# Kernel tuning notes

Hardware: AMD Instinct MI355X
Metric: run time of the kernel (lower is better)

## Reference

```python
import jax, jax.numpy as jnp
import numpy as np

N, E = 100000, 1600000
IN_DIM, EDGE_DIM, H, D = 128, 16, 8, 16
SLOPE = 0.2


def setup_inputs() -> dict:
    key = jax.random.key(0)
    k1, k2, k3, k4, k5, k6, k7 = jax.random.split(key, 7)
    node_embeddings = jax.random.normal(k1, (N, IN_DIM), dtype=jnp.float32)
    edge_index = jax.random.randint(k2, (2, E), 0, N, dtype=jnp.int64)
    edge_features = jax.random.normal(k3, (E, EDGE_DIM), dtype=jnp.float32)
    # xavier_uniform with gain 1/sqrt(2) for linear weights (shape [out, in])
    g = 1.0 / np.sqrt(2.0)
    b_node = g * np.sqrt(6.0 / (IN_DIM + H * D))
    W_node = jax.random.uniform(k4, (H * D, IN_DIM), jnp.float32, -b_node, b_node)
    b_edge = g * np.sqrt(6.0 / (EDGE_DIM + H * D))
    W_edge = jax.random.uniform(k5, (H * D, EDGE_DIM), jnp.float32, -b_edge, b_edge)
    # xavier on attn_vec.unsqueeze(0): fan_in = 3D, fan_out = H*3D? torch treats
    # (1, H, 3D) as fan_in=3D, fan_out=H*3D is not standard; torch uses last dim as fan_in,
    # dims[-2]=H as fan_out for 3D tensors with receptive field 1 -> fan_in=3D, fan_out=H.
    b_a = np.sqrt(6.0 / (H + 3 * D))
    attn_vec = jax.random.uniform(k6, (H, 3 * D), jnp.float32, -b_a, b_a)
    return {
        "node_embeddings": node_embeddings,
        "edge_features": edge_features,
        "W_node": W_node,
        "W_edge": W_edge,
        "attn_vec": attn_vec,
        "edge_index": edge_index,
    }


def _leaky_relu(x, slope=SLOPE):
    return jnp.where(x >= 0, x, slope * x)


def reference(node_embeddings, edge_features, W_node, W_edge, attn_vec, edge_index):
    n = node_embeddings.shape[0]
    src, dst = edge_index[0], edge_index[1]
    h = (node_embeddings @ W_node.T).reshape(n, H, D)           # (N,H,D)
    ef = (edge_features @ W_edge.T).reshape(-1, H, D)           # (E,H,D)
    a_src, a_dst, a_edge = attn_vec[:, :D], attn_vec[:, D:2 * D], attn_vec[:, 2 * D:]
    # split the dot product: a^T [h_src || h_dst || e] = a1.h_src + a2.h_dst + a3.e
    s_node_src = jnp.einsum('nhd,hd->nh', h, a_src)             # (N,H)
    s_node_dst = jnp.einsum('nhd,hd->nh', h, a_dst)             # (N,H)
    score = s_node_src[src] + s_node_dst[dst] + jnp.einsum('ehd,hd->eh', ef, a_edge)
    score = _leaky_relu(score)                                  # (E,H)
    # torch scatter_reduce amax with include_self=True on zeros init => max(seg_max, 0)
    seg_max = jnp.maximum(jax.ops.segment_max(score, dst, num_segments=n), 0.0)  # (N,H)
    exp_s = jnp.exp(score - seg_max[dst])                       # (E,H)
    denom = jax.ops.segment_sum(exp_s, dst, num_segments=n)     # (N,H)
    w = exp_s / (denom[dst] + 1e-9)                             # (E,H)  (dropout in eval mode)
    msg = h[src] * w[:, :, None]                                # (E,H,D)
    out = jax.ops.segment_sum(msg, dst, num_segments=n)         # (N,H,D)
    return jax.nn.elu(out).reshape(n, H * D)
```

## Files before the change

### kernel.cpp

```cpp
#include <hip/hip_runtime.h>
#include <hip/hip_bf16.h>
#include <hip/hip_fp16.h>
#include <math.h>

#define NN 100000
#define NE 1600000
#define SLOPE 0.2f
#define BSH 9
#define NB 196
#define BCAP 10240
#define CLDS 10752
#define EPB 4096
#define NTB 64

typedef float  f32x4 __attribute__((ext_vector_type(4)));
typedef unsigned int u32x4 __attribute__((ext_vector_type(4)));
typedef _Float16 half8 __attribute__((ext_vector_type(8)));
typedef float floatx4 __attribute__((ext_vector_type(4)));

__global__ __launch_bounds__(128) void prep_v_kernel(
    const float* __restrict__ W_edge, const float* __restrict__ attn,
    float* __restrict__ v)
{
    int t = threadIdx.x;
    int h = t >> 4, k = t & 15;
    float acc = 0.f;
#pragma unroll
    for (int d = 0; d < 16; ++d)
        acc += attn[h * 48 + 32 + d] * W_edge[(h * 16 + d) * 16 + k];
    v[t] = acc;
}

__global__ __launch_bounds__(256) void node_transform(
    const float* __restrict__ X, const float* __restrict__ Wn,
    const float* __restrict__ attn, __half* __restrict__ h_fp,
    float* __restrict__ s_src, float* __restrict__ s_dst)
{
    __shared__ _Float16 Wl[128 * 128];

    int t = threadIdx.x;
#pragma unroll
    for (int it = 0; it < 8; ++it) {
        int gid = t + it * 256;
        int j  = gid >> 4;
        int gk = gid & 15;
        const float4* wp = reinterpret_cast<const float4*>(Wn + (size_t)j * 128 + gk * 8);
        float4 w0 = wp[0], w1 = wp[1];
        half8 hw;
        hw[0] = (_Float16)w0.x; hw[1] = (_Float16)w0.y;
        hw[2] = (_Float16)w0.z; hw[3] = (_Float16)w0.w;
        hw[4] = (_Float16)w1.x; hw[5] = (_Float16)w1.y;
        hw[6] = (_Float16)w1.z; hw[7] = (_Float16)w1.w;
        int sg = gk ^ (j & 7);
        *reinterpret_cast<half8*>(&Wl[j * 128 + sg * 8]) = hw;
    }
    __syncthreads();

    int lane = t & 63;
    int wave = t >> 6;
    int c = lane & 15;
    int g = lane >> 4;
    int n0 = blockIdx.x * NTB + wave * 16;
    if (n0 >= NN) return;

    floatx4 acc[8];
#pragma unroll
    for (int jt = 0; jt < 8; ++jt) acc[jt] = (floatx4){0.f, 0.f, 0.f, 0.f};

    const float4* xrow = reinterpret_cast<const float4*>(X + (size_t)(n0 + c) * 128);
#pragma unroll
    for (int kb = 0; kb < 4; ++kb) {
        float4 x0 = xrow[kb * 8 + g * 2];
        float4 x1 = xrow[kb * 8 + g * 2 + 1];
        half8 a;
        a[0] = (_Float16)x0.x; a[1] = (_Float16)x0.y;
        a[2] = (_Float16)x0.z; a[3] = (_Float16)x0.w;
        a[4] = (_Float16)x1.x; a[5] = (_Float16)x1.y;
        a[6] = (_Float16)x1.z; a[7] = (_Float16)x1.w;
#pragma unroll
        for (int jt = 0; jt < 8; ++jt) {
            int sg = (kb * 4 + g) ^ (c & 7);
            half8 b = *reinterpret_cast<const half8*>(&Wl[(jt * 16 + c) * 128 + sg * 8]);
            acc[jt] = __builtin_amdgcn_mfma_f32_16x16x32_f16(a, b, acc[jt], 0, 0, 0);
        }
    }

    float as_l[8], ad_l[8];
#pragma unroll
    for (int jt = 0; jt < 8; ++jt) {
        as_l[jt] = attn[jt * 48 + c];
        ad_l[jt] = attn[jt * 48 + 16 + c];
    }

#pragma unroll
    for (int jt = 0; jt < 8; ++jt) {
#pragma unroll
        for (int r = 0; r < 4; ++r) {
            float hv = acc[jt][r];
            int node = n0 + g * 4 + r;
            h_fp[(size_t)node * 128 + jt * 16 + c] = __float2half_rn(hv);
            float p1 = hv * as_l[jt];
            float p2 = hv * ad_l[jt];
#pragma unroll
            for (int m = 1; m < 16; m <<= 1) {
                p1 += __shfl_xor(p1, m);
                p2 += __shfl_xor(p2, m);
            }
            if (c == 0) {
                s_src[(size_t)node * 8 + jt] = p1;
                s_dst[(size_t)node * 8 + jt] = p2;
            }
        }
    }
}

__global__ __launch_bounds__(256) void edge_score_partition(
    const int* __restrict__ ei, const float* __restrict__ ef,
    const float* __restrict__ vglob, const float* __restrict__ s_src,
    const float* __restrict__ s_dst, unsigned int* __restrict__ bcursor,
    u32x4* __restrict__ esc4, u32x4* __restrict__ esc_s,
    int2* __restrict__ brec)
{
    __shared__ float v[128];
    __shared__ unsigned int hist[256];
    __shared__ unsigned int runstart[256];
    __shared__ unsigned int cursor[256];
    __shared__ unsigned int gbase[NB];
    __shared__ int           sdst[EPB];
    __shared__ int           ssin[EPB];
    __shared__ unsigned int  skey[EPB];
    __shared__ unsigned int  ssrc[EPB];
    __shared__ unsigned short sbkt[EPB];

    int t = threadIdx.x;
    int e0 = blockIdx.x * EPB;
    int ecnt = min(EPB, NE - e0);

    if (t < 128) v[t] = vglob[t];
    hist[t] = 0;
    __syncthreads();

    const f32x4* ef4 = reinterpret_cast<const f32x4*>(ef);
    const float4* ss4 = reinterpret_cast<const float4*>(s_src);
    const float4* sd4 = reinterpret_cast<const float4*>(s_dst);

    for (int i = t; i < ecnt; i += 256) {
        int e = e0 + i;
        int src = ei[e];
        int dst = ei[NE + e];
        sdst[i] = dst;
        ssin[i] = src;
        atomicAdd(&hist[dst >> BSH], 1u);

        float tt[8] = {0.f, 0.f, 0.f, 0.f, 0.f, 0.f, 0.f, 0.f};
#pragma unroll
        for (int r = 0; r < 4; ++r) {
            f32x4 fv = ef4[(size_t)e * 4 + r];
#pragma unroll
            for (int hh = 0; hh < 8; ++hh) {
                tt[hh] += fv[0] * v[hh * 16 + r * 4 + 0]
                        + fv[1] * v[hh * 16 + r * 4 + 1]
                        + fv[2] * v[hh * 16 + r * 4 + 2]
                        + fv[3] * v[hh * 16 + r * 4 + 3];
            }
        }
        float4 a0 = ss4[(size_t)src * 2], a1 = ss4[(size_t)src * 2 + 1];
        float4 b0 = sd4[(size_t)dst * 2], b1 = sd4[(size_t)dst * 2 + 1];
        float sa[8] = {a0.x, a0.y, a0.z, a0.w, a1.x, a1.y, a1.z, a1.w};
        float sb[8] = {b0.x, b0.y, b0.z, b0.w, b1.x, b1.y, b1.z, b1.w};
        u32x4 pk4;
#pragma unroll
        for (int hp = 0; hp < 4; ++hp) {
            unsigned int lohi[2];
#pragma unroll
            for (int half_ = 0; half_ < 2; ++half_) {
                int hh = hp * 2 + half_;
                float s = sa[hh] + sb[hh] + tt[hh];
                s = (s >= 0.f) ? s : SLOPE * s;
                lohi[half_] = (unsigned int)__half_as_ushort(__float2half_rn(__expf(s)));
            }
            pk4[hp] = lohi[0] | (lohi[1] << 16);
        }
        esc4[e] = pk4;
    }
    __syncthreads();

    unsigned int hv = hist[t];
    runstart[t] = hv;
    __syncthreads();
    for (int o = 1; o < 256; o <<= 1) {
        unsigned int u = (t >= o) ? runstart[t - o] : 0u;
        __syncthreads();
        runstart[t] += u;
        __syncthreads();
    }
    unsigned int excl = runstart[t] - hv;
    __syncthreads();
    runstart[t] = excl;
    cursor[t] = excl;
    if (t < NB) gbase[t] = atomicAdd(&bcursor[t], hv);
    __syncthreads();

    for (int i = t; i < ecnt; i += 256) {
        int e = e0 + i;
        int dst = sdst[i];
        int b = dst >> BSH;
        unsigned int slot = atomicAdd(&cursor[b], 1u);
        skey[slot] = ((unsigned int)e << BSH) | (unsigned int)(dst & 511);
        ssrc[slot] = (unsigned int)ssin[i];
        sbkt[slot] = (unsigned short)b;
    }
    __syncthreads();

    for (int s = t; s < ecnt; s += 256) {
        int b = sbkt[s];
        unsigned int gpos = gbase[b] + ((unsigned int)s - runstart[b]);
        if (gpos < BCAP) {
            unsigned int key = skey[s];
            unsigned int e = key >> BSH;
            brec[(size_t)b * BCAP + gpos] =
                make_int2((int)((gpos << BSH) | (key & 511u)), (int)ssrc[s]);
            esc_s[(size_t)b * BCAP + gpos] = esc4[e];
        }
    }
}

__global__ __launch_bounds__(512) void bucket_sort(
    const unsigned int* __restrict__ bcursor, int2* __restrict__ brec,
    uint2* __restrict__ noff)
{
    __shared__ unsigned int ncnt[512];
    __shared__ unsigned int offL[513];
    __shared__ unsigned int ncur[512];
    __shared__ unsigned int se[CLDS];
    __shared__ unsigned int ss[CLDS];

    int t = threadIdx.x;
    int b = blockIdx.x;
    int n0 = b << BSH;
    unsigned int cnt = bcursor[b];
    if (cnt > BCAP) cnt = BCAP;
    int2* rin = brec + (size_t)b * BCAP;

    ncnt[t] = 0;
    __syncthreads();
    for (unsigned int i = t; i < cnt; i += 512)
        atomicAdd(&ncnt[(unsigned int)rin[i].x & 511u], 1u);
    __syncthreads();
    unsigned int ec = (ncnt[t] + 1u) & ~1u;
    offL[t] = ec;
    __syncthreads();
    for (int o = 1; o < 512; o <<= 1) {
        unsigned int u = (t >= o) ? offL[t - o] : 0u;
        __syncthreads();
        offL[t] += u;
        __syncthreads();
    }
    unsigned int incl = offL[t];
    unsigned int excl = incl - ec;
    __syncthreads();
    offL[t] = excl;
    ncur[t] = 0;
    if (t == 511) offL[512] = incl;
    __syncthreads();
    for (unsigned int i = t; i < cnt; i += 512) {
        int2 r = rin[i];
        unsigned int key = (unsigned int)r.x;
        unsigned int ld = key & 511u;
        unsigned int pos = atomicAdd(&ncur[ld], 1u);
        unsigned int slot = offL[ld] + pos;
        if (slot < CLDS) {
            se[slot] = key >> BSH;
            ss[slot] = (unsigned int)r.y;
        }
    }
    __syncthreads();
    unsigned int total = offL[512];
    if (total > BCAP) total = BCAP;
    for (unsigned int s = t; s < total; s += 512)
        rin[s] = make_int2((int)se[s], (int)ss[s]);
    int n = n0 + t;
    if (n < NN)
        noff[n] = make_uint2((unsigned int)b * BCAP + offL[t], ncnt[t]);
}

__global__ __launch_bounds__(256) void node_aggregate(
    const uint2* __restrict__ noff, const int2* __restrict__ perm2,
    const __half* __restrict__ esc_s, const __half* __restrict__ h_fp,
    float* __restrict__ out)
{
    int lane = threadIdx.x & 63;
    int n = blockIdx.x * (blockDim.x >> 6) + (threadIdx.x >> 6);
    if (n >= NN) return;
    int q = lane >> 3;
    const unsigned int* hl = reinterpret_cast<const unsigned int*>(h_fp) + lane;
    const __half* el = esc_s + ((size_t)(n >> BSH) * BCAP) * 8 + q;

    uint2 oc = noff[n];
    unsigned int s0 = oc.x, s1 = s0 + oc.y;
    float denom = 0.f, a0 = 0.f, a1 = 0.f;
    unsigned int i = s0;

    for (; i + 8 <= s1; i += 8) {
        int4 pa = *reinterpret_cast<const int4*>(&perm2[i]);
        int4 pb = *reinterpret_cast<const int4*>(&perm2[i + 2]);
        int4 pc = *reinterpret_cast<const int4*>(&perm2[i + 4]);
        int4 pd = *reinterpret_cast<const int4*>(&perm2[i + 6]);
        unsigned int u0 = hl[(size_t)pa.y * 64];
        unsigned int u1 = hl[(size_t)pa.w * 64];
        unsigned int u2 = hl[(size_t)pb.y * 64];
        unsigned int u3 = hl[(size_t)pb.w * 64];
        unsigned int u4 = hl[(size_t)pc.y * 64];
        unsigned int u5 = hl[(size_t)pc.w * 64];
        unsigned int u6 = hl[(size_t)pd.y * 64];
        unsigned int u7 = hl[(size_t)pd.w * 64];
        float e0 = __half2float(el[(size_t)pa.x * 8]);
        float e1 = __half2float(el[(size_t)pa.z * 8]);
        float e2 = __half2float(el[(size_t)pb.x * 8]);
        float e3 = __half2float(el[(size_t)pb.z * 8]);
        float e4 = __half2float(el[(size_t)pc.x * 8]);
        float e5 = __half2float(el[(size_t)pc.z * 8]);
        float e6 = __half2float(el[(size_t)pd.x * 8]);
        float e7 = __half2float(el[(size_t)pd.z * 8]);
        float2 h0 = __half22float2(*reinterpret_cast<const __half2*>(&u0));
        float2 h1 = __half22float2(*reinterpret_cast<const __half2*>(&u1));
        float2 h2 = __half22float2(*reinterpret_cast<const __half2*>(&u2));
        float2 h3 = __half22float2(*reinterpret_cast<const __half2*>(&u3));
        float2 h4 = __half22float2(*reinterpret_cast<const __half2*>(&u4));
        float2 h5 = __half22float2(*reinterpret_cast<const __half2*>(&u5));
        float2 h6 = __half22float2(*reinterpret_cast<const __half2*>(&u6));
        float2 h7 = __half22float2(*reinterpret_cast<const __half2*>(&u7));
        denom += ((e0 + e1) + (e2 + e3)) + ((e4 + e5) + (e6 + e7));
        a0 = fmaf(h0.x, e0, a0); a0 = fmaf(h1.x, e1, a0);
        a0 = fmaf(h2.x, e2, a0); a0 = fmaf(h3.x, e3, a0);
        a0 = fmaf(h4.x, e4, a0); a0 = fmaf(h5.x, e5, a0);
        a0 = fmaf(h6.x, e6, a0); a0 = fmaf(h7.x, e7, a0);
        a1 = fmaf(h0.y, e0, a1); a1 = fmaf(h1.y, e1, a1);
        a1 = fmaf(h2.y, e2, a1); a1 = fmaf(h3.y, e3, a1);
        a1 = fmaf(h4.y, e4, a1); a1 = fmaf(h5.y, e5, a1);
        a1 = fmaf(h6.y, e6, a1); a1 = fmaf(h7.y, e7, a1);
    }
    for (; i + 4 <= s1; i += 4) {
        int4 pa = *reinterpret_cast<const int4*>(&perm2[i]);
        int4 pb = *reinterpret_cast<const int4*>(&perm2[i + 2]);
        unsigned int u0 = hl[(size_t)pa.y * 64];
        unsigned int u1 = hl[(size_t)pa.w * 64];
        unsigned int u2 = hl[(size_t)pb.y * 64];
        unsigned int u3 = hl[(size_t)pb.w * 64];
        float e0 = __half2float(el[(size_t)pa.x * 8]);
        float e1 = __half2float(el[(size_t)pa.z * 8]);
        float e2 = __half2float(el[(size_t)pb.x * 8]);
        float e3 = __half2float(el[(size_t)pb.z * 8]);
        float2 h0 = __half22float2(*reinterpret_cast<const __half2*>(&u0));
        float2 h1 = __half22float2(*reinterpret_cast<const __half2*>(&u1));
        float2 h2 = __half22float2(*reinterpret_cast<const __half2*>(&u2));
        float2 h3 = __half22float2(*reinterpret_cast<const __half2*>(&u3));
        denom += (e0 + e1) + (e2 + e3);
        a0 = fmaf(h0.x, e0, a0); a0 = fmaf(h1.x, e1, a0);
        a0 = fmaf(h2.x, e2, a0); a0 = fmaf(h3.x, e3, a0);
        a1 = fmaf(h0.y, e0, a1); a1 = fmaf(h1.y, e1, a1);
        a1 = fmaf(h2.y, e2, a1); a1 = fmaf(h3.y, e3, a1);
    }
    for (; i < s1; ++i) {
        int2 p = perm2[i];
        unsigned int u = hl[(size_t)p.y * 64];
        float e = __half2float(el[(size_t)p.x * 8]);
        float2 hf = __half22float2(*reinterpret_cast<const __half2*>(&u));
        denom += e;
        a0 = fmaf(hf.x, e, a0);
        a1 = fmaf(hf.y, e, a1);
    }

    float w = 1.f / (denom + 1e-9f);
    a0 *= w; a1 *= w;
    a0 = a0 > 0.f ? a0 : expm1f(a0);
    a1 = a1 > 0.f ? a1 : expm1f(a1);
    reinterpret_cast<float2*>(out)[(size_t)n * 64 + lane] = make_float2(a0, a1);
}

extern "C" void kernel_launch(void* const* d_in, const int* in_sizes, int n_in,
                              void* d_out, int out_size, void* d_ws, size_t ws_size,
                              hipStream_t stream)
{
    const float* X    = (const float*)d_in[0];
    const float* EF   = (const float*)d_in[1];
    const float* Wn   = (const float*)d_in[2];
    const float* We   = (const float*)d_in[3];
    const float* attn = (const float*)d_in[4];
    const int*   ei   = (const int*)d_in[5];
    float* out = (float*)d_out;

    char* ws = (char*)d_ws;
    int2*   brec  = (int2*)ws;
    u32x4*  esc4  = (u32x4*)(brec + (size_t)NB * BCAP);
    u32x4*  esc_s = esc4 + NE;
    float*  s_src = (float*)(esc_s + (size_t)NB * BCAP);
    float*  s_dst = s_src + (size_t)NN * 8;
    float*  vbuf  = s_dst + (size_t)NN * 8;
    unsigned int* bcursor = (unsigned int*)(vbuf + 128);
    uint2*  noff  = (uint2*)(bcursor + 256);
    __half* h_fp  = (__half*)(noff + NN);

    hipMemsetAsync(bcursor, 0, 256 * sizeof(unsigned int), stream);

    prep_v_kernel<<<1, 128, 0, stream>>>(We, attn, vbuf);
    node_transform<<<(NN + NTB - 1) / NTB, 256, 0, stream>>>(X, Wn, attn, h_fp,
                                                             s_src, s_dst);
    edge_score_partition<<<(NE + EPB - 1) / EPB, 256, 0, stream>>>(
        ei, EF, vbuf, s_src, s_dst, bcursor, esc4, esc_s, brec);
    bucket_sort<<<NB, 512, 0, stream>>>(bcursor, brec, noff);
    node_aggregate<<<(NN + 3) / 4, 256, 0, stream>>>(noff, brec,
                                                     (const __half*)esc_s,
                                                     h_fp, out);
}
```

Before: 224.5 us.

## Compute bucket slots before scoring and write scores directly to bucketed positions

Edge-score partitioning now builds the histogram and prefix scan before computing scores. Each edge grabs its bucket slot via an LDS atomic, and its packed fp16 scores are written straight into the bucketed esc_s array. This removes the intermediate esc4 buffer (a 16-byte store plus a later gather read per edge) and the LDS staging of sorted keys. The trade-off is that edge index reads and score computation fall into separate passes, and the output writes within each bucket are less contiguous than the old slot-ordered scatter.

```diff
diff --git a/kernel.cpp b/kernel.cpp
--- a/kernel.cpp
+++ b/kernel.cpp
@@ -118,8 +118,7 @@
     const int* __restrict__ ei, const float* __restrict__ ef,
     const float* __restrict__ vglob, const float* __restrict__ s_src,
     const float* __restrict__ s_dst, unsigned int* __restrict__ bcursor,
-    u32x4* __restrict__ esc4, u32x4* __restrict__ esc_s,
-    int2* __restrict__ brec)
+    u32x4* __restrict__ esc_s, int2* __restrict__ brec)
 {
     __shared__ float v[128];
     __shared__ unsigned int hist[256];
@@ -128,9 +127,6 @@
     __shared__ unsigned int gbase[NB];
     __shared__ int           sdst[EPB];
     __shared__ int           ssin[EPB];
-    __shared__ unsigned int  skey[EPB];
-    __shared__ unsigned int  ssrc[EPB];
-    __shared__ unsigned short sbkt[EPB];
 
     int t = threadIdx.x;
     int e0 = blockIdx.x * EPB;
@@ -140,17 +136,46 @@
     hist[t] = 0;
     __syncthreads();
 
+    for (int i = t; i < ecnt; i += 256) {
+        int src = ei[e0 + i];
+        int dst = ei[NE + e0 + i];
+        sdst[i] = dst;
+        ssin[i] = src;
+        atomicAdd(&hist[dst >> BSH], 1u);
+    }
+    __syncthreads();
+
+    unsigned int hv = hist[t];
+    runstart[t] = hv;
+    __syncthreads();
+    for (int o = 1; o < 256; o <<= 1) {
+        unsigned int u = (t >= o) ? runstart[t - o] : 0u;
+        __syncthreads();
+        runstart[t] += u;
+        __syncthreads();
+    }
+    unsigned int excl = runstart[t] - hv;
+    __syncthreads();
+    runstart[t] = excl;
+    cursor[t] = excl;
+    if (t < NB) gbase[t] = atomicAdd(&bcursor[t], hv);
+    __syncthreads();
+
     const f32x4* ef4 = reinterpret_cast<const f32x4*>(ef);
     const float4* ss4 = reinterpret_cast<const float4*>(s_src);
     const float4* sd4 = reinterpret_cast<const float4*>(s_dst);
 
     for (int i = t; i < ecnt; i += 256) {
         int e = e0 + i;
-        int src = ei[e];
-        int dst = ei[NE + e];
-        sdst[i] = dst;
-        ssin[i] = src;
-        atomicAdd(&hist[dst >> BSH], 1u);
+        int dst = sdst[i];
+        int src = ssin[i];
+        int b = dst >> BSH;
+        unsigned int slot = atomicAdd(&cursor[b], 1u);
+        unsigned int gp = gbase[b] + (slot - runstart[b]);
+        bool ok = (gp < BCAP);
+        if (ok)
+            brec[(size_t)b * BCAP + gp] =
+                make_int2((int)((gp << BSH) | (unsigned int)(dst & 511)), src);
 
         float tt[8] = {0.f, 0.f, 0.f, 0.f, 0.f, 0.f, 0.f, 0.f};
 #pragma unroll
@@ -181,47 +206,8 @@
             }
             pk4[hp] = lohi[0] | (lohi[1] << 16);
         }
-        esc4[e] = pk4;
-    }
-    __syncthreads();
-
-    unsigned int hv = hist[t];
-    runstart[t] = hv;
-    __syncthreads();
-    for (int o = 1; o < 256; o <<= 1) {
-        unsigned int u = (t >= o) ? runstart[t - o] : 0u;
-        __syncthreads();
-        runstart[t] += u;
-        __syncthreads();
-    }
-    unsigned int excl = runstart[t] - hv;
-    __syncthreads();
-    runstart[t] = excl;
-    cursor[t] = excl;
-    if (t < NB) gbase[t] = atomicAdd(&bcursor[t], hv);
-    __syncthreads();
-
-    for (int i = t; i < ecnt; i += 256) {
-        int e = e0 + i;
-        int dst = sdst[i];
-        int b = dst >> BSH;
-        unsigned int slot = atomicAdd(&cursor[b], 1u);
-        skey[slot] = ((unsigned int)e << BSH) | (unsigned int)(dst & 511);
-        ssrc[slot] = (unsigned int)ssin[i];
-        sbkt[slot] = (unsigned short)b;
-    }
-    __syncthreads();
-
-    for (int s = t; s < ecnt; s += 256) {
-        int b = sbkt[s];
-        unsigned int gpos = gbase[b] + ((unsigned int)s - runstart[b]);
-        if (gpos < BCAP) {
-            unsigned int key = skey[s];
-            unsigned int e = key >> BSH;
-            brec[(size_t)b * BCAP + gpos] =
-                make_int2((int)((gpos << BSH) | (key & 511u)), (int)ssrc[s]);
-            esc_s[(size_t)b * BCAP + gpos] = esc4[e];
-        }
+        if (ok)
+            esc_s[(size_t)b * BCAP + gp] = pk4;
     }
 }
 
@@ -392,8 +378,7 @@
 
     char* ws = (char*)d_ws;
     int2*   brec  = (int2*)ws;
-    u32x4*  esc4  = (u32x4*)(brec + (size_t)NB * BCAP);
-    u32x4*  esc_s = esc4 + NE;
+    u32x4*  esc_s = (u32x4*)(brec + (size_t)NB * BCAP);
     float*  s_src = (float*)(esc_s + (size_t)NB * BCAP);
     float*  s_dst = s_src + (size_t)NN * 8;
     float*  vbuf  = s_dst + (size_t)NN * 8;
@@ -407,7 +392,7 @@
     node_transform<<<(NN + NTB - 1) / NTB, 256, 0, stream>>>(X, Wn, attn, h_fp,
                                                              s_src, s_dst);
     edge_score_partition<<<(NE + EPB - 1) / EPB, 256, 0, stream>>>(
-        ei, EF, vbuf, s_src, s_dst, bcursor, esc4, esc_s, brec);
+        ei, EF, vbuf, s_src, s_dst, bcursor, esc_s, brec);
     bucket_sort<<<NB, 512, 0, stream>>>(bcursor, brec, noff);
     node_aggregate<<<(NN + 3) / 4, 256, 0, stream>>>(noff, brec,
                                                      (const __half*)esc_s,
```

Measured after the change: 265.5 us. 18.2% more time.
